# Performance work log

Measured on AMD Instinct MI355X. Metric: run time of the kernel, lower is better.

The kernel has to match this reference:

```python
import jax, jax.numpy as jnp
import numpy as np
from jax import lax

N, CI, CO, K, H, W_SP, M = 32, 256, 256, 3, 64, 64, 4
TAU = 1.0 / 30.0
PAD = 1  # spatial-preserving for k=3, stride=1, dilation=1


def setup_inputs() -> dict:
    key = jax.random.key(0)
    ks = jax.random.split(key, 6)
    # kaiming_normal fan_out for the kernel bank: fan_out = CO*K*K (per torch semantics on this 6D tensor layout)
    fan_out = CO * K * K
    std = np.sqrt(2.0 / fan_out)
    x = jax.random.normal(ks[0], (N, CI, H, W_SP), dtype=jnp.float32)
    Wbank = jax.random.normal(ks[1], (CO, M, CI, K, K), dtype=jnp.float32) * std
    Bbank = jnp.zeros((CO, M), dtype=jnp.float32)
    hid = CI // M  # att_fc hidden = in_channels // num_weights
    w1 = jax.random.normal(ks[2], (hid, CI), dtype=jnp.float32) * np.sqrt(1.0 / CI)
    b1 = jnp.zeros((hid,), dtype=jnp.float32)
    w2 = jax.random.normal(ks[3], (M, hid), dtype=jnp.float32) * np.sqrt(1.0 / hid)
    b2 = jnp.zeros((M,), dtype=jnp.float32)
    return {"x": x, "Wbank": Wbank, "Bbank": Bbank, "w1": w1, "b1": b1, "w2": w2, "b2": b2}


def reference(x, Wbank, Bbank, w1, b1, w2, b2):
    n, ci, h, w = x.shape
    co = Wbank.shape[0]
    # attention over kernels: global avg pool -> 1x1 conv MLP -> softmax(logits * tau)
    pooled = jnp.mean(x, axis=(2, 3))                      # N,Ci
    hmid = jax.nn.relu(pooled @ w1.T + b1)                 # N,hid
    logits = hmid @ w2.T + b2                              # N,M
    pi = jax.nn.softmax(logits * TAU, axis=1)              # N,M
    # per-sample aggregated kernels and biases
    wn = jnp.einsum("nm,omikl->noikl", pi, Wbank)          # N,Co,Ci,K,K
    bn = pi @ Bbank.T                                      # N,Co
    # batch-as-groups conv2d (spatial-preserving)
    xg = x.reshape(1, n * ci, h, w)
    wg = wn.reshape(n * co, ci, K, K)
    y = lax.conv_general_dilated(
        xg, wg,
        window_strides=(1, 1),
        padding=[(PAD, PAD), (PAD, PAD)],
        rhs_dilation=(1, 1),
        dimension_numbers=("NCHW", "OIHW", "NCHW"),
        feature_group_count=n,
    )
    y = y.reshape(n, co, h, w) + bn[:, :, None, None]
    return y
```

## Files before the change

### kernel.cpp

```cpp
#include <hip/hip_runtime.h>
#include <hip/hip_bf16.h>
#include <stdint.h>

typedef __bf16 bf16;
typedef __bf16 bf16x8 __attribute__((ext_vector_type(8)));
typedef float f32x4 __attribute__((ext_vector_type(4)));

#define TAU (1.0f/30.0f)

#define NB 32
#define CI 256
#define CO 256
#define HH 64
#define WW 64
#define HID 64

#define WN_ELEMS ((size_t)NB*8*9*16*512)
#define WN_BYTES (WN_ELEMS*2)
#define XB_ELEMS ((size_t)NB*32*64*64*8)
#define XB_BYTES (XB_ELEMS*2)

__device__ __forceinline__ void async16(void* lds_uniform_base, const void* g_perlane) {
  __builtin_amdgcn_global_load_lds(
      (const __attribute__((address_space(1))) uint32_t*)g_perlane,
      (__attribute__((address_space(3))) uint32_t*)lds_uniform_base, 16, 0, 0);
}

__global__ void cvt_pool_kernel(const float* __restrict__ x, bf16* __restrict__ xb,
                                float* __restrict__ pooled) {
  const int cg = blockIdx.x, n = blockIdx.y, tid = threadIdx.x;
  const float* base = x + ((size_t)n*CI + cg*8)*4096;
  bf16* ob = xb + ((size_t)n*32 + cg)*4096*8;
  float s[8];
#pragma unroll
  for (int j = 0; j < 8; ++j) s[j] = 0.f;
  for (int it = 0; it < 16; ++it) {
    int pos = it*256 + tid;
    bf16x8 o;
#pragma unroll
    for (int j = 0; j < 8; ++j) {
      float v = base[(size_t)j*4096 + pos];
      s[j] += v;
      o[j] = (bf16)v;
    }
    *(bf16x8*)(ob + (size_t)pos*8) = o;
  }
  __shared__ float red[4][8];
#pragma unroll
  for (int j = 0; j < 8; ++j)
#pragma unroll
    for (int off = 32; off; off >>= 1) s[j] += __shfl_xor(s[j], off);
  int wv = tid >> 6, lane = tid & 63;
  if (lane == 0)
#pragma unroll
    for (int j = 0; j < 8; ++j) red[wv][j] = s[j];
  __syncthreads();
  if (tid < 8) {
    float t = red[0][tid] + red[1][tid] + red[2][tid] + red[3][tid];
    pooled[n*CI + cg*8 + tid] = t * (1.0f/4096.0f);
  }
}

__global__ void attn_kernel(const float* __restrict__ pooled,
                            const float* __restrict__ w1, const float* __restrict__ b1,
                            const float* __restrict__ w2, const float* __restrict__ b2,
                            float* __restrict__ pi) {
  int n = blockIdx.x, h = threadIdx.x;
  __shared__ float hm[HID];
  __shared__ float lgs[4];
  const float* pr = pooled + n*CI;
  float s = b1[h];
  for (int c = 0; c < CI; ++c) s += pr[c] * w1[h*CI + c];
  hm[h] = s > 0.f ? s : 0.f;
  __syncthreads();
  if (h < 4) {
    float lg = b2[h];
    for (int k = 0; k < HID; ++k) lg += hm[k] * w2[h*HID + k];
    lgs[h] = lg * TAU;
  }
  __syncthreads();
  if (h == 0) {
    float mx = fmaxf(fmaxf(lgs[0], lgs[1]), fmaxf(lgs[2], lgs[3]));
    float e0 = expf(lgs[0]-mx), e1 = expf(lgs[1]-mx), e2 = expf(lgs[2]-mx), e3 = expf(lgs[3]-mx);
    float inv = 1.f / (e0+e1+e2+e3);
    pi[n*4+0] = e0*inv; pi[n*4+1] = e1*inv; pi[n*4+2] = e2*inv; pi[n*4+3] = e3*inv;
  }
}

__global__ void agg_kernel(const float* __restrict__ Wbank, const float* __restrict__ pi,
                           bf16* __restrict__ wn) {
  int wid = blockIdx.x * 4 + (threadIdx.x >> 6);
  int lane = threadIdx.x & 63;
  int c = wid / 144;
  int rem = wid - c*144;
  int kk = rem >> 4;
  int cbg = rem & 15;
  int co  = cbg*16 + (lane & 15);
  int ci0 = c*32 + (lane >> 4)*8;
  float w[4][8];
#pragma unroll
  for (int m = 0; m < 4; ++m)
#pragma unroll
    for (int j = 0; j < 8; ++j)
      w[m][j] = Wbank[(size_t)((co*4 + m)*256 + ci0 + j)*9 + kk];
  for (int n = 0; n < NB; ++n) {
    float p0 = pi[n*4+0], p1 = pi[n*4+1], p2 = pi[n*4+2], p3 = pi[n*4+3];
    bf16x8 o;
#pragma unroll
    for (int j = 0; j < 8; ++j)
      o[j] = (bf16)(p0*w[0][j] + p1*w[1][j] + p2*w[2][j] + p3*w[3][j]);
    *(bf16x8*)(wn + ((size_t)n*1152 + c*144 + kk*16 + cbg)*512 + lane*8) = o;
  }
}

#define XROWS 10
#define XW 66
#define XS_E (4*XROWS*XW*8)

__global__ __launch_bounds__(256, 2)
void conv_kernel(const bf16* __restrict__ xb, const bf16* __restrict__ wn,
                 const float* __restrict__ pi, const float* __restrict__ Bbank,
                 float* __restrict__ y) {
  __shared__ __align__(16) bf16 xs[XS_E];
  __shared__ float bns[64];
  const int tid = threadIdx.x;
  const int wv = tid >> 6, lane = tid & 63;
  const int l = lane & 15, u = lane >> 4;
  const int flat = blockIdx.x;
  const int wid = ((flat & 7) << 7) + (flat >> 3);
  const int n   = wid >> 5;
  const int hwb = (wid >> 2) & 7;
  const int cot = wid & 3;
  const int h0 = hwb * 8;

  for (int i = tid; i < XS_E/8; i += 256) ((int4*)xs)[i] = int4{0,0,0,0};
  if (tid < 64) {
    int co = cot*64 + tid;
    bns[tid] = pi[n*4+0]*Bbank[co*4+0] + pi[n*4+1]*Bbank[co*4+1]
             + pi[n*4+2]*Bbank[co*4+2] + pi[n*4+3]*Bbank[co*4+3];
  }

  f32x4 acc[2][4][4];
#pragma unroll
  for (int o = 0; o < 2; ++o)
#pragma unroll
    for (int a = 0; a < 4; ++a)
#pragma unroll
      for (int b = 0; b < 4; ++b)
#pragma unroll
        for (int k = 0; k < 4; ++k) acc[o][a][b][k] = 0.f;

  const bf16* wnb = wn + (size_t)n * 1152 * 512 + (size_t)cot*4*512 + lane*8;
  const bf16* xgb = xb + (size_t)n*32*4096*8 + lane*8;

  for (int c = 0; c < 8; ++c) {
    __syncthreads();
    {
      const bf16* xg = xgb + (size_t)(c*4 + wv)*4096*8;
#pragma unroll
      for (int r = 0; r < XROWS; ++r) {
        int hp = h0 - 1 + r;
        if (hp >= 0 && hp < HH)
          async16(&xs[((wv*XROWS + r)*XW + 1)*8], xg + (size_t)hp*64*8);
      }
    }
    __syncthreads();
    const bf16* wc = wnb + (size_t)c*144*512;
#pragma unroll
    for (int kx = 0; kx < 3; ++kx) {
      bf16x8 bfr[4][4];
#pragma unroll
      for (int rr = 0; rr < 4; ++rr)
#pragma unroll
        for (int f = 0; f < 4; ++f)
          bfr[rr][f] = *(const bf16x8*)(&xs[((u*XROWS + wv*2 + rr)*XW + f*16 + l + kx)*8]);
#pragma unroll
      for (int ky = 0; ky < 3; ++ky) {
        const int kk = ky*3 + kx;
        bf16x8 afr[4];
#pragma unroll
        for (int cb = 0; cb < 4; ++cb)
          afr[cb] = *(const bf16x8*)(wc + (size_t)(kk*16 + cb)*512);
#pragma unroll
        for (int cb = 0; cb < 4; ++cb)
#pragma unroll
          for (int o = 0; o < 2; ++o)
#pragma unroll
            for (int f = 0; f < 4; ++f)
              acc[o][cb][f] = __builtin_amdgcn_mfma_f32_16x16x32_bf16(afr[cb], bfr[o+ky][f], acc[o][cb][f], 0, 0, 0);
      }
    }
  }
#pragma unroll
  for (int o = 0; o < 2; ++o) {
    const int h = h0 + wv*2 + o;
#pragma unroll
    for (int cb = 0; cb < 4; ++cb) {
#pragma unroll
      for (int f = 0; f < 4; ++f) {
        const int wcol = f*16 + l;
#pragma unroll
        for (int r4 = 0; r4 < 4; ++r4) {
          const int col = cb*16 + u*4 + r4;
          y[(((size_t)n*CO + cot*64 + col)*HH + h)*WW + wcol] = acc[o][cb][f][r4] + bns[col];
        }
      }
    }
  }
}

extern "C" void kernel_launch(void* const* d_in, const int* in_sizes, int n_in,
                              void* d_out, int out_size, void* d_ws, size_t ws_size,
                              hipStream_t stream) {
  const float* x     = (const float*)d_in[0];
  const float* Wbank = (const float*)d_in[1];
  const float* Bbank = (const float*)d_in[2];
  const float* w1    = (const float*)d_in[3];
  const float* b1    = (const float*)d_in[4];
  const float* w2    = (const float*)d_in[5];
  const float* b2    = (const float*)d_in[6];
  float* y = (float*)d_out;

  bf16*  wn     = (bf16*)d_ws;
  bf16*  xb     = (bf16*)((char*)d_ws + WN_BYTES);
  float* pooled = (float*)((char*)d_ws + WN_BYTES + XB_BYTES);
  float* pi     = pooled + NB*CI;

  dim3 cg(32, NB);
  cvt_pool_kernel<<<cg, 256, 0, stream>>>(x, xb, pooled);
  attn_kernel<<<NB, HID, 0, stream>>>(pooled, w1, b1, w2, b2, pi);
  agg_kernel<<<288, 256, 0, stream>>>(Wbank, pi, wn);
  conv_kernel<<<1024, 256, 0, stream>>>(xb, wn, pi, Bbank, y);
}
```

Before: 199.3 us.

## Stage conv weights through LDS with register prefetch and rotating input rows

Each wave now cooperatively loads one quarter of the per-chunk weight fragments into registers, prefetches the next chunk's weights while the current chunk computes, and writes them into a shared LDS buffer instead of every wave reading all weight fragments from global memory. The input-row fragments are rotated through two register sets across ky instead of holding a 4x4 array, and MFMA bursts get raised wave priority. This cuts redundant global weight traffic and register pressure, but adds about 36KB of LDS per block, which may limit the two-blocks-per-CU occupancy target and adds LDS bandwidth pressure.

```diff
diff --git a/kernel.cpp b/kernel.cpp
--- a/kernel.cpp
+++ b/kernel.cpp
@@ -116,12 +116,14 @@
 #define XROWS 10
 #define XW 66
 #define XS_E (4*XROWS*XW*8)
+#define WA_E (9*4*512)
 
 __global__ __launch_bounds__(256, 2)
 void conv_kernel(const bf16* __restrict__ xb, const bf16* __restrict__ wn,
                  const float* __restrict__ pi, const float* __restrict__ Bbank,
                  float* __restrict__ y) {
   __shared__ __align__(16) bf16 xs[XS_E];
+  __shared__ __align__(16) bf16 wa[WA_E];
   __shared__ float bns[64];
   const int tid = threadIdx.x;
   const int wv = tid >> 6, lane = tid & 63;
@@ -133,6 +135,19 @@
   const int cot = wid & 3;
   const int h0 = hwb * 8;
 
+  const bf16* wnb = wn + (size_t)n*1152*512 + (size_t)(cot*4 + wv)*512 + lane*8;
+  const bf16* xgb = xb + (size_t)n*32*4096*8 + lane*8;
+
+  bf16x8 wstg[9];
+  auto LOADW = [&](int c) {
+    const bf16* seg = wnb + (size_t)c*144*512;
+#pragma unroll
+    for (int kk = 0; kk < 9; ++kk)
+      wstg[kk] = *(const bf16x8*)(seg + (size_t)kk*16*512);
+  };
+
+  LOADW(0);
+
   for (int i = tid; i < XS_E/8; i += 256) ((int4*)xs)[i] = int4{0,0,0,0};
   if (tid < 64) {
     int co = cot*64 + tid;
@@ -150,9 +165,6 @@
 #pragma unroll
         for (int k = 0; k < 4; ++k) acc[o][a][b][k] = 0.f;
 
-  const bf16* wnb = wn + (size_t)n * 1152 * 512 + (size_t)cot*4*512 + lane*8;
-  const bf16* xgb = xb + (size_t)n*32*4096*8 + lane*8;
-
   for (int c = 0; c < 8; ++c) {
     __syncthreads();
     {
@@ -164,31 +176,41 @@
           async16(&xs[((wv*XROWS + r)*XW + 1)*8], xg + (size_t)hp*64*8);
       }
     }
+#pragma unroll
+    for (int kk = 0; kk < 9; ++kk)
+      *(int4*)(&wa[kk*2048 + wv*512 + lane*8]) = *(int4*)&wstg[kk];
     __syncthreads();
-    const bf16* wc = wnb + (size_t)c*144*512;
+    if (c < 7) LOADW(c + 1);
+
+    auto LD = [&](int rr, int f, int kx) {
+      return *(const bf16x8*)(&xs[((u*XROWS + wv*2 + rr)*XW + f*16 + l + kx)*8]);
+    };
+    auto MM = [&](int ky, int kx, bf16x8 (&lo)[4], bf16x8 (&hi)[4]) {
+      const int kk = ky*3 + kx;
+      __builtin_amdgcn_s_setprio(1);
+#pragma unroll
+      for (int cb = 0; cb < 4; ++cb) {
+        bf16x8 afr = *(const bf16x8*)(&wa[kk*2048 + cb*512 + lane*8]);
+#pragma unroll
+        for (int f = 0; f < 4; ++f) {
+          acc[0][cb][f] = __builtin_amdgcn_mfma_f32_16x16x32_bf16(afr, lo[f], acc[0][cb][f], 0, 0, 0);
+          acc[1][cb][f] = __builtin_amdgcn_mfma_f32_16x16x32_bf16(afr, hi[f], acc[1][cb][f], 0, 0, 0);
+        }
+      }
+      __builtin_amdgcn_s_setprio(0);
+    };
 #pragma unroll
     for (int kx = 0; kx < 3; ++kx) {
-      bf16x8 bfr[4][4];
-#pragma unroll
-      for (int rr = 0; rr < 4; ++rr)
-#pragma unroll
-        for (int f = 0; f < 4; ++f)
-          bfr[rr][f] = *(const bf16x8*)(&xs[((u*XROWS + wv*2 + rr)*XW + f*16 + l + kx)*8]);
-#pragma unroll
-      for (int ky = 0; ky < 3; ++ky) {
-        const int kk = ky*3 + kx;
-        bf16x8 afr[4];
-#pragma unroll
-        for (int cb = 0; cb < 4; ++cb)
-          afr[cb] = *(const bf16x8*)(wc + (size_t)(kk*16 + cb)*512);
-#pragma unroll
-        for (int cb = 0; cb < 4; ++cb)
-#pragma unroll
-          for (int o = 0; o < 2; ++o)
-#pragma unroll
-            for (int f = 0; f < 4; ++f)
-              acc[o][cb][f] = __builtin_amdgcn_mfma_f32_16x16x32_bf16(afr[cb], bfr[o+ky][f], acc[o][cb][f], 0, 0, 0);
-      }
+      bf16x8 rA[4], rB[4];
+#pragma unroll
+      for (int f = 0; f < 4; ++f) { rA[f] = LD(0, f, kx); rB[f] = LD(1, f, kx); }
+      MM(0, kx, rA, rB);
+#pragma unroll
+      for (int f = 0; f < 4; ++f) rA[f] = LD(2, f, kx);
+      MM(1, kx, rB, rA);
+#pragma unroll
+      for (int f = 0; f < 4; ++f) rB[f] = LD(3, f, kx);
+      MM(2, kx, rA, rB);
     }
   }
 #pragma unroll
```

After: 189.2 us. 1.05x faster.

## Pre-pad input planes and stream weights through double-buffered LDS in conv

Applied to the files above, without the earlier changes.

The bf16 conversion kernel now writes each input plane with a zero halo (66x66), so the conv kernel can read activation fragments straight from global memory with no bounds checks and no LDS staging. Weights, which were read from global inside the loop, are now staged asynchronously into a double-buffered LDS area, prefetching the next channel chunk while the current one is computed. Global activation loads are interleaved with MFMA groups under raised wave priority. The exchange is more global-memory traffic for activations, which now rely on cache reuse, plus a larger padded workspace.

```diff
diff --git a/kernel.cpp b/kernel.cpp
--- a/kernel.cpp
+++ b/kernel.cpp
@@ -17,7 +17,8 @@
 
 #define WN_ELEMS ((size_t)NB*8*9*16*512)
 #define WN_BYTES (WN_ELEMS*2)
-#define XB_ELEMS ((size_t)NB*32*64*64*8)
+#define PLANE_E 34848
+#define XB_ELEMS ((size_t)NB*32*PLANE_E)
 #define XB_BYTES (XB_ELEMS*2)
 
 __device__ __forceinline__ void async16(void* lds_uniform_base, const void* g_perlane) {
@@ -30,12 +31,21 @@
                                 float* __restrict__ pooled) {
   const int cg = blockIdx.x, n = blockIdx.y, tid = threadIdx.x;
   const float* base = x + ((size_t)n*CI + cg*8)*4096;
-  bf16* ob = xb + ((size_t)n*32 + cg)*4096*8;
+  bf16* ob = xb + ((size_t)n*32 + cg)*PLANE_E;
+  for (int i = tid; i < 260; i += 256) {
+    int hr, wl;
+    if (i < 66)       { hr = 0;       wl = i; }
+    else if (i < 132) { hr = 65;      wl = i - 66; }
+    else if (i < 196) { hr = i - 131; wl = 0; }
+    else              { hr = i - 195; wl = 65; }
+    *(int4*)(ob + ((size_t)hr*66 + wl)*8) = int4{0,0,0,0};
+  }
   float s[8];
 #pragma unroll
   for (int j = 0; j < 8; ++j) s[j] = 0.f;
   for (int it = 0; it < 16; ++it) {
     int pos = it*256 + tid;
+    int h = pos >> 6, w = pos & 63;
     bf16x8 o;
 #pragma unroll
     for (int j = 0; j < 8; ++j) {
@@ -43,7 +53,7 @@
       s[j] += v;
       o[j] = (bf16)v;
     }
-    *(bf16x8*)(ob + (size_t)pos*8) = o;
+    *(bf16x8*)(ob + ((size_t)(h+1)*66 + (w+1))*8) = o;
   }
   __shared__ float red[4][8];
 #pragma unroll
@@ -113,15 +123,31 @@
   }
 }
 
-#define XROWS 10
-#define XW 66
-#define XS_E (4*XROWS*XW*8)
+#define WA_E (9*4*512)
+
+#define LDG(st, rr, kxx, cc) { _Pragma("unroll") \
+  for (int f = 0; f < 4; ++f) \
+    S[st][f] = *(const bf16x8*)(xu + ((size_t)(cc)*139392 + (rr)*528 + f*128 + (kxx)*8)); }
+
+#define MM(kkv, lo, hi) { \
+  __builtin_amdgcn_s_setprio(1); \
+  _Pragma("unroll") for (int cb = 0; cb < 4; ++cb) { \
+    bf16x8 afr = *(const bf16x8*)(&wab[(kkv)*2048 + cb*512 + lane*8]); \
+    _Pragma("unroll") for (int f = 0; f < 4; ++f) { \
+      acc[0][cb][f] = __builtin_amdgcn_mfma_f32_16x16x32_bf16(afr, lo[f], acc[0][cb][f], 0,0,0); \
+      acc[1][cb][f] = __builtin_amdgcn_mfma_f32_16x16x32_bf16(afr, hi[f], acc[1][cb][f], 0,0,0); \
+    } } \
+  __builtin_amdgcn_s_setprio(0); }
+
+#define STAGE_W(cc, b) { const bf16* seg = wnb + (size_t)(cc)*73728; \
+  _Pragma("unroll") for (int kk = 0; kk < 9; ++kk) \
+    async16(&wa[b][kk*2048 + wv*512], seg + (size_t)kk*8192); }
 
 __global__ __launch_bounds__(256, 2)
 void conv_kernel(const bf16* __restrict__ xb, const bf16* __restrict__ wn,
                  const float* __restrict__ pi, const float* __restrict__ Bbank,
                  float* __restrict__ y) {
-  __shared__ __align__(16) bf16 xs[XS_E];
+  __shared__ __align__(16) bf16 wa[2][WA_E];
   __shared__ float bns[64];
   const int tid = threadIdx.x;
   const int wv = tid >> 6, lane = tid & 63;
@@ -133,7 +159,11 @@
   const int cot = wid & 3;
   const int h0 = hwb * 8;
 
-  for (int i = tid; i < XS_E/8; i += 256) ((int4*)xs)[i] = int4{0,0,0,0};
+  const bf16* wnb = wn + (size_t)n*1152*512 + (size_t)(cot*4 + wv)*512 + lane*8;
+  const bf16* xu = xb + (((size_t)(n*32 + u)*66 + (h0 + wv*2))*66 + l)*8;
+
+  STAGE_W(0, 0);
+
   if (tid < 64) {
     int co = cot*64 + tid;
     bns[tid] = pi[n*4+0]*Bbank[co*4+0] + pi[n*4+1]*Bbank[co*4+1]
@@ -150,46 +180,21 @@
 #pragma unroll
         for (int k = 0; k < 4; ++k) acc[o][a][b][k] = 0.f;
 
-  const bf16* wnb = wn + (size_t)n * 1152 * 512 + (size_t)cot*4*512 + lane*8;
-  const bf16* xgb = xb + (size_t)n*32*4096*8 + lane*8;
-
   for (int c = 0; c < 8; ++c) {
     __syncthreads();
-    {
-      const bf16* xg = xgb + (size_t)(c*4 + wv)*4096*8;
-#pragma unroll
-      for (int r = 0; r < XROWS; ++r) {
-        int hp = h0 - 1 + r;
-        if (hp >= 0 && hp < HH)
-          async16(&xs[((wv*XROWS + r)*XW + 1)*8], xg + (size_t)hp*64*8);
-      }
-    }
-    __syncthreads();
-    const bf16* wc = wnb + (size_t)c*144*512;
-#pragma unroll
-    for (int kx = 0; kx < 3; ++kx) {
-      bf16x8 bfr[4][4];
-#pragma unroll
-      for (int rr = 0; rr < 4; ++rr)
-#pragma unroll
-        for (int f = 0; f < 4; ++f)
-          bfr[rr][f] = *(const bf16x8*)(&xs[((u*XROWS + wv*2 + rr)*XW + f*16 + l + kx)*8]);
-#pragma unroll
-      for (int ky = 0; ky < 3; ++ky) {
-        const int kk = ky*3 + kx;
-        bf16x8 afr[4];
-#pragma unroll
-        for (int cb = 0; cb < 4; ++cb)
-          afr[cb] = *(const bf16x8*)(wc + (size_t)(kk*16 + cb)*512);
-#pragma unroll
-        for (int cb = 0; cb < 4; ++cb)
-#pragma unroll
-          for (int o = 0; o < 2; ++o)
-#pragma unroll
-            for (int f = 0; f < 4; ++f)
-              acc[o][cb][f] = __builtin_amdgcn_mfma_f32_16x16x32_bf16(afr[cb], bfr[o+ky][f], acc[o][cb][f], 0, 0, 0);
-      }
-    }
+    if (c < 7) STAGE_W(c + 1, (c + 1) & 1);
+    const bf16* wab = wa[c & 1];
+    bf16x8 S[4][4];
+    LDG(0, 0, 0, c) LDG(1, 1, 0, c) LDG(2, 2, 0, c) LDG(3, 3, 0, c)
+    MM(0, S[0], S[1])
+    MM(3, S[1], S[2]) LDG(0, 0, 1, c) LDG(1, 1, 1, c)
+    MM(6, S[2], S[3]) LDG(2, 2, 1, c)
+    MM(1, S[0], S[1]) LDG(3, 3, 1, c)
+    MM(4, S[1], S[2]) LDG(0, 0, 2, c) LDG(1, 1, 2, c)
+    MM(7, S[2], S[3]) LDG(2, 2, 2, c)
+    MM(2, S[0], S[1]) LDG(3, 3, 2, c)
+    MM(5, S[1], S[2])
+    MM(8, S[2], S[3])
   }
 #pragma unroll
   for (int o = 0; o < 2; ++o) {
```

After: 191.9 us. -3.7%, faster.
